# Performance work log

Measured on AMD Instinct MI355X. Metric: run time of the kernel, lower is better.

The kernel has to match this reference:

```python
import jax, jax.numpy as jnp
import numpy as np

ALPHA = 0.34          # Ewald splitting parameter (init kwarg alpha)
MAX_HKL = 12          # init kwarg max_hkl
TWO_PI = 2.0 * np.pi


def setup_inputs() -> dict:
    key = jax.random.key(0)
    k1, k2 = jax.random.split(key)
    N = 4096
    L = 40.0  # cubic box edge (Angstrom)
    coords = jax.random.uniform(k1, (N, 3), dtype=jnp.float32) * L
    q = jax.random.normal(k2, (N,), dtype=jnp.float32)
    q = q - jnp.mean(q)  # neutral cell (k=0 term is excluded)
    box = jnp.eye(3, dtype=jnp.float32) * L
    return {"coords": coords, "box": box, "q": q}


def _ewald_recip_energy(coords, box, q):
    """Reciprocal-space Ewald sum over |h|,|k|,|l| <= MAX_HKL (rank=0 PME fallback).

    pot_i = (4*pi/V) * sum_{k!=0} exp(-|k|^2/(4 a^2))/|k|^2 * Re[S(k) exp(-i k.r_i)]
    E     = 0.5 * sum_i q_i * pot_i
    """
    K = MAX_HKL
    vol = jnp.abs(jnp.linalg.det(box))
    recip = TWO_PI * jnp.linalg.inv(box).T  # rows = reciprocal lattice vectors (3,3)
    h = jnp.arange(-K, K + 1)
    hh, kk, ll = jnp.meshgrid(h, h, h, indexing="ij")
    hkl = jnp.stack([hh.ravel(), kk.ravel(), ll.ravel()], axis=-1).astype(jnp.float32)  # (Nk,3)
    kvecs = hkl @ recip                      # (Nk,3)
    k2 = jnp.sum(kvecs * kvecs, axis=-1)     # (Nk,)
    nonzero = k2 > 0.0                       # mask out k = 0 (static shape, jit-safe)
    k2_safe = jnp.where(nonzero, k2, 1.0)
    inv_4a2 = 1.0 / (4.0 * ALPHA * ALPHA)
    fac = jnp.where(nonzero, jnp.exp(-k2_safe * inv_4a2) / k2_safe, 0.0)  # (Nk,)
    phases = coords @ kvecs.T                # (N, Nk)
    c = jnp.cos(phases)
    s = jnp.sin(phases)
    Sre = q @ c                              # (Nk,) Re S(k)
    Sim = q @ s                              # (Nk,) Im S(k)
    pref = (4.0 * np.pi) / vol
    # Re[S(k) e^{-i k.r_i}] = Sre*cos + Sim*sin
    pot = pref * (c @ (fac * Sre) + s @ (fac * Sim))  # (N,)
    return 0.5 * jnp.sum(q * pot)


def reference(coords, box, q):
    return _ewald_recip_energy(coords, box, q)
```

## Files before the change

### kernel.cpp

```cpp
#include <hip/hip_runtime.h>
#include <math.h>

namespace {
constexpr int   KMAX   = 12;
constexpr int   NLINE  = 313;
constexpr int   NGROUP = NLINE * 5;
constexpr int   NKV    = NGROUP * 5;
constexpr int   NSLICE = 4;
constexpr int   SLICE_CAP = 512;
constexpr int   S2_BLOCKS = (NKV + 255) / 256;
constexpr float ALPHA_  = 0.34f;
constexpr float TWO_PI_ = 6.283185307179586f;
}

__device__ __forceinline__ void cofactors(const float* __restrict__ box,
                                          float C[3][3], float* det) {
  const float b00 = box[0], b01 = box[1], b02 = box[2];
  const float b10 = box[3], b11 = box[4], b12 = box[5];
  const float b20 = box[6], b21 = box[7], b22 = box[8];
  C[0][0] =  (b11 * b22 - b12 * b21);
  C[0][1] = -(b10 * b22 - b12 * b20);
  C[0][2] =  (b10 * b21 - b11 * b20);
  C[1][0] = -(b01 * b22 - b02 * b21);
  C[1][1] =  (b00 * b22 - b02 * b20);
  C[1][2] = -(b00 * b21 - b01 * b20);
  C[2][0] =  (b01 * b12 - b02 * b11);
  C[2][1] = -(b00 * b12 - b02 * b10);
  C[2][2] =  (b00 * b11 - b01 * b10);
  *det = b00 * C[0][0] + b01 * C[0][1] + b02 * C[0][2];
}

__device__ __forceinline__ void line_hk(int L, int* h, int* k) {
  if (L < 300)      { *h = L / 25 + 1; *k = L % 25 - 12; }
  else if (L < 312) { *h = 0;          *k = L - 299;     }
  else              { *h = 0;          *k = 0;           }
}

__global__ __launch_bounds__(256, 6) void ewald_g5(
    const float* __restrict__ coords, const float* __restrict__ box,
    const float* __restrict__ q, int N, float2* __restrict__ partial)
{
  __shared__ float4 sf4[SLICE_CAP];
  __shared__ float2 sf2[SLICE_CAP];

  float C[3][3], det;
  cofactors(box, C, &det);
  const float invdet = 1.0f / det;

  const int slice = blockIdx.y;
  const int sp    = (N + NSLICE - 1) / NSLICE;
  const int s_beg = slice * sp;
  const int s_end = min(s_beg + sp, N);

  const int lane = threadIdx.x & 63;
  const int g    = blockIdx.x * 4 + (threadIdx.x >> 6);
  const int gc   = (g < NGROUP) ? g : (NGROUP - 1);

  int h, k; line_hk(gc / 5, &h, &k);
  const float hf  = (float)h;
  const float kf  = (float)k;
  const float l0f = (float)(-KMAX + 5 * (gc % 5));

  float Sre[5] = {0.f, 0.f, 0.f, 0.f, 0.f};
  float Sim[5] = {0.f, 0.f, 0.f, 0.f, 0.f};

  for (int cb = s_beg; cb < s_end; cb += SLICE_CAP) {
    const int cnt = min(SLICE_CAP, s_end - cb);
    __syncthreads();
    for (int t = threadIdx.x; t < SLICE_CAP; t += 256) {
      float4 v4 = make_float4(0.f, 0.f, 1.f, 0.f);
      float2 v2 = make_float2(0.f, 0.f);
      if (t < cnt) {
        const int gi = cb + t;
        const float x = coords[3 * gi + 0];
        const float y = coords[3 * gi + 1];
        const float z = coords[3 * gi + 2];
        v4.x = (x * C[0][0] + y * C[0][1] + z * C[0][2]) * invdet;
        v4.y = (x * C[1][0] + y * C[1][1] + z * C[1][2]) * invdet;
        float c = (x * C[2][0] + y * C[2][1] + z * C[2][2]) * invdet;
        c = c - floorf(c);
        float cr, sr;
        asm("v_sin_f32 %0, %1" : "=v"(sr) : "v"(c));
        asm("v_cos_f32 %0, %1" : "=v"(cr) : "v"(c));
        v4.z = cr; v4.w = sr;
        v2.x = c;  v2.y = q[gi];
      }
      sf4[t] = v4; sf2[t] = v2;
    }
    __syncthreads();

#pragma unroll 2
    for (int i = lane; i < SLICE_CAP; i += 64) {
      const float4 p = sf4[i];
      const float2 w = sf2[i];
      float t0 = fmaf(hf, p.x, fmaf(kf, p.y, l0f * w.x));
      float tf;
      asm("v_fract_f32 %0, %1" : "=v"(tf) : "v"(t0));
      float s0, c0;
      asm("v_sin_f32 %0, %1" : "=v"(s0) : "v"(tf));
      asm("v_cos_f32 %0, %1" : "=v"(c0) : "v"(tf));
      float Pre = w.y * c0, Pim = w.y * s0;
      Sre[0] += Pre; Sim[0] += Pim;
      const float cr = p.z, sr = p.w;
#pragma unroll
      for (int u = 1; u < 5; ++u) {
        const float nre = fmaf(Pre, cr, -(Pim * sr));
        const float nim = fmaf(Pre, sr,  (Pim * cr));
        Pre = nre; Pim = nim;
        Sre[u] += Pre; Sim[u] += Pim;
      }
    }
  }

#pragma unroll
  for (int off = 32; off > 0; off >>= 1) {
#pragma unroll
    for (int u = 0; u < 5; ++u) {
      Sre[u] += __shfl_xor(Sre[u], off);
      Sim[u] += __shfl_xor(Sim[u], off);
    }
  }

  if (g < NGROUP && lane == 0) {
#pragma unroll
    for (int u = 0; u < 5; ++u) {
      partial[(size_t)(g * 5 + u) * NSLICE + slice] = make_float2(Sre[u], Sim[u]);
    }
  }
}

__global__ __launch_bounds__(256) void stage2(
    const float2* __restrict__ partial, const float* __restrict__ box,
    float* __restrict__ out)
{
  __shared__ float red[256];
  const int idx = blockIdx.x * 256 + threadIdx.x;
  float e = 0.f;
  if (idx < NKV) {
    const int g = idx / 5, u = idx % 5;
    const int line = g / 5;
    const int l = -KMAX + 5 * (g % 5) + u;
    int h, k; line_hk(line, &h, &k);
    if (!(h == 0 && k == 0 && l <= 0)) {
      float re = 0.f, im = 0.f;
      for (int s = 0; s < NSLICE; ++s) {
        const float2 p = partial[(size_t)idx * NSLICE + s];
        re += p.x; im += p.y;
      }
      float C[3][3], det;
      cofactors(box, C, &det);
      const float invdet = 1.0f / det;
      const float hf = (float)h, kf = (float)k, lf = (float)l;
      const float kx = (hf * C[0][0] + kf * C[1][0] + lf * C[2][0]) * invdet;
      const float ky = (hf * C[0][1] + kf * C[1][1] + lf * C[2][1]) * invdet;
      const float kz = (hf * C[0][2] + kf * C[1][2] + lf * C[2][2]) * invdet;
      const float k2 = TWO_PI_ * TWO_PI_ * (kx * kx + ky * ky + kz * kz);
      const float fac = __expf(-k2 / (4.0f * ALPHA_ * ALPHA_)) / k2;
      e = fac * fmaf(re, re, im * im);
    }
  }
  red[threadIdx.x] = e;
  __syncthreads();
  for (int s = 128; s > 0; s >>= 1) {
    if (threadIdx.x < s) red[threadIdx.x] += red[threadIdx.x + s];
    __syncthreads();
  }
  if (threadIdx.x == 0) {
    float C[3][3], det;
    cofactors(box, C, &det);
    const float scale = (4.0f * 3.14159265358979323846f) / fabsf(det);
    atomicAdd(out, scale * red[0]);
  }
}

extern "C" void kernel_launch(void* const* d_in, const int* in_sizes, int n_in,
                              void* d_out, int out_size, void* d_ws, size_t ws_size,
                              hipStream_t stream) {
  const float* coords = (const float*)d_in[0];
  const float* box    = (const float*)d_in[1];
  const float* q      = (const float*)d_in[2];
  float* out = (float*)d_out;
  const int N = in_sizes[2];

  float2* partial = (float2*)d_ws;

  hipMemsetAsync(out, 0, sizeof(float), stream);
  const dim3 grid((NGROUP + 3) / 4, NSLICE);
  hipLaunchKernelGGL(ewald_g5, grid, dim3(256), 0, stream,
                     coords, box, q, N, partial);
  hipLaunchKernelGGL(stage2, dim3(S2_BLOCKS), dim3(256), 0, stream,
                     partial, box, out);
}
```

Before: 24.15 us.

## Double atom slices, fold output zeroing into main kernel, raise unroll

Raises the number of atom slices from 4 to 8, which doubles the grid and gives each block half as many atoms. The output memset is replaced by zeroing inside the first kernel, removing one stream operation. The inner loop unroll goes from 2 to 4 and the occupancy hint in launch bounds is dropped. The warp reduction switches to shuffle-down, and stage2 now reads twice as many partials per k-vector.

```diff
diff --git a/kernel.cpp b/kernel.cpp
--- a/kernel.cpp
+++ b/kernel.cpp
@@ -6,7 +6,7 @@
 constexpr int   NLINE  = 313;
 constexpr int   NGROUP = NLINE * 5;
 constexpr int   NKV    = NGROUP * 5;
-constexpr int   NSLICE = 4;
+constexpr int   NSLICE = 8;
 constexpr int   SLICE_CAP = 512;
 constexpr int   S2_BLOCKS = (NKV + 255) / 256;
 constexpr float ALPHA_  = 0.34f;
@@ -36,12 +36,15 @@
   else              { *h = 0;          *k = 0;           }
 }
 
-__global__ __launch_bounds__(256, 6) void ewald_g5(
+__global__ __launch_bounds__(256) void ewald_groups(
     const float* __restrict__ coords, const float* __restrict__ box,
-    const float* __restrict__ q, int N, float2* __restrict__ partial)
+    const float* __restrict__ q, int N, float2* __restrict__ partial,
+    float* __restrict__ out)
 {
   __shared__ float4 sf4[SLICE_CAP];
   __shared__ float2 sf2[SLICE_CAP];
+
+  if (blockIdx.x == 0 && blockIdx.y == 0 && threadIdx.x == 0) out[0] = 0.0f;
 
   float C[3][3], det;
   cofactors(box, C, &det);
@@ -89,7 +92,7 @@
     }
     __syncthreads();
 
-#pragma unroll 2
+#pragma unroll 4
     for (int i = lane; i < SLICE_CAP; i += 64) {
       const float4 p = sf4[i];
       const float2 w = sf2[i];
@@ -116,16 +119,14 @@
   for (int off = 32; off > 0; off >>= 1) {
 #pragma unroll
     for (int u = 0; u < 5; ++u) {
-      Sre[u] += __shfl_xor(Sre[u], off);
-      Sim[u] += __shfl_xor(Sim[u], off);
+      Sre[u] += __shfl_down(Sre[u], off);
+      Sim[u] += __shfl_down(Sim[u], off);
     }
   }
-
   if (g < NGROUP && lane == 0) {
 #pragma unroll
-    for (int u = 0; u < 5; ++u) {
+    for (int u = 0; u < 5; ++u)
       partial[(size_t)(g * 5 + u) * NSLICE + slice] = make_float2(Sre[u], Sim[u]);
-    }
   }
 }
 
@@ -138,15 +139,14 @@
   float e = 0.f;
   if (idx < NKV) {
     const int g = idx / 5, u = idx % 5;
-    const int line = g / 5;
-    const int l = -KMAX + 5 * (g % 5) + u;
-    int h, k; line_hk(line, &h, &k);
+    const int L = g / 5, sub = g % 5;
+    int h, k; line_hk(L, &h, &k);
+    const int l = -KMAX + 5 * sub + u;
     if (!(h == 0 && k == 0 && l <= 0)) {
       float re = 0.f, im = 0.f;
-      for (int s = 0; s < NSLICE; ++s) {
-        const float2 p = partial[(size_t)idx * NSLICE + s];
-        re += p.x; im += p.y;
-      }
+      const float2* p = partial + (size_t)idx * NSLICE;
+#pragma unroll
+      for (int s = 0; s < NSLICE; ++s) { re += p[s].x; im += p[s].y; }
       float C[3][3], det;
       cofactors(box, C, &det);
       const float invdet = 1.0f / det;
@@ -184,10 +184,9 @@
 
   float2* partial = (float2*)d_ws;
 
-  hipMemsetAsync(out, 0, sizeof(float), stream);
   const dim3 grid((NGROUP + 3) / 4, NSLICE);
-  hipLaunchKernelGGL(ewald_g5, grid, dim3(256), 0, stream,
-                     coords, box, q, N, partial);
+  hipLaunchKernelGGL(ewald_groups, grid, dim3(256), 0, stream,
+                     coords, box, q, N, partial, out);
   hipLaunchKernelGGL(stage2, dim3(S2_BLOCKS), dim3(256), 0, stream,
                      partial, box, out);
 }
```

Measured after the change: 21.12 us. -12.5%, faster.
